# Performance work log

Measured on AMD Instinct MI355X. Metric: run time of the kernel, lower is better.

The kernel has to match this reference:

```python
import jax, jax.numpy as jnp
import numpy as np

N = 262144
IN_DIM = 1024
HID = 256
E = 16
TOP_K = 2


def setup_inputs() -> dict:
    key = jax.random.key(0)
    k1, k2, k3, k4, k5 = jax.random.split(key, 5)
    x = jax.random.normal(k1, (N, IN_DIM), dtype=jnp.float32)
    # Kaiming-ish init scaled for stability
    W1 = jax.random.normal(k2, (IN_DIM, HID), dtype=jnp.float32) * (1.0 / np.sqrt(IN_DIM))
    b1 = jnp.zeros((HID,), dtype=jnp.float32)
    W2 = jax.random.normal(k3, (HID, E), dtype=jnp.float32) * (1.0 / np.sqrt(HID))
    b2 = jnp.zeros((E,), dtype=jnp.float32)
    return {"x": x, "W1": W1, "b1": b1, "W2": W2, "b2": b2}


def reference(x, W1, b1, W2, b2):
    # MLP router: Linear -> ELU -> Linear
    h = jax.nn.elu(x @ W1 + b1)            # [N, HID]
    logits = h @ W2 + b2                   # [N, E]
    # top-k mask: keep top-k logits, set the rest to -inf (scatter semantics)
    vals, idx = jax.lax.top_k(logits, TOP_K)          # [N, K]
    rows = jnp.arange(logits.shape[0])[:, None]        # [N, 1]
    masked = jnp.full_like(logits, -jnp.inf).at[rows, idx].set(vals)
    alpha = jax.nn.softmax(masked, axis=-1)            # [N, E]
    return alpha, logits
```

## Files before the change

### kernel.cpp

```cpp
#include <hip/hip_runtime.h>
#include <math.h>

#define KDIM 1024
#define HID 256
#define NE 16
#define ROWS_BLK 128
#define KCH 32
#define NCHUNK 32
#define CH_BYTES 32768
#define W2T_PLANE (NE * HID)
#define ABUF(i) ((i) * 16384)
#define SMEM_BYTES 65536

typedef __attribute__((ext_vector_type(8))) _Float16 f16x8;
typedef __attribute__((ext_vector_type(16))) float f32x16;
typedef __attribute__((ext_vector_type(4))) float f32x4;

__global__ void prep_w1(const float* __restrict__ W1, _Float16* __restrict__ img) {
  int idx = blockIdx.x * 256 + threadIdx.x;
  int col = idx & 255, kgl = idx >> 8;
  int c = kgl >> 2, kg = kgl & 3, k8 = kgl * 8;
  f16x8 p1, p2;
#pragma unroll
  for (int i = 0; i < 8; ++i) {
    float v = W1[(size_t)(k8 + i) * HID + col];
    _Float16 a = (_Float16)v;
    _Float16 b = (_Float16)((v - (float)a) * 4096.0f);
    p1[i] = a; p2[i] = b;
  }
  size_t off = (size_t)c * 16384 + (size_t)kg * 2048 + (size_t)col * 8;
  *(f16x8*)(img + off) = p1;
  *(f16x8*)(img + off + 8192) = p2;
}

__global__ void prep_w2(const float* __restrict__ W2, _Float16* __restrict__ w2t) {
  int idx = blockIdx.x * 256 + threadIdx.x;
  int e = idx & 15, k = idx >> 4;
  float v = W2[(size_t)k * NE + e];
  _Float16 a = (_Float16)v;
  _Float16 b = (_Float16)((v - (float)a) * 4096.0f);
  w2t[(size_t)e * HID + k] = a;
  w2t[W2T_PLANE + (size_t)e * HID + k] = b;
}

__global__ __launch_bounds__(512, 2) void fused_router(
    const float* __restrict__ x, const _Float16* __restrict__ w1img,
    const _Float16* __restrict__ w2t, const float* __restrict__ bias1,
    const float* __restrict__ bias2, float* __restrict__ outA,
    float* __restrict__ outL)
{
  extern __shared__ char smem[];
  const int t = threadIdx.x, l = t & 63, w = t >> 6;
  const int rowg = w >> 2, colg = w & 3;
  const int l31 = l & 31, hi = l >> 5;
  const int R0 = blockIdx.x * ROWS_BLK;
  const int arow0 = rowg * 64 + l31;
  const int bcol0 = colg * 64 + l31;

  const int xr = t >> 2, xq = t & 3;
  const float* xbase = x + (size_t)(R0 + xr) * KDIM + xq * 8;

  const char* bimg = (const char*)w1img + (size_t)bcol0 * 16 + (size_t)hi * 4096;

  f32x16 acc0[2][2], accA[2][2];
#pragma unroll
  for (int rt = 0; rt < 2; ++rt)
#pragma unroll
    for (int ct = 0; ct < 2; ++ct)
#pragma unroll
      for (int j = 0; j < 16; ++j) { acc0[rt][ct][j] = 0.f; accA[rt][ct][j] = 0.f; }

  float xvA[8], xvB[8];
  f16x8 bsetA[8], bsetB[8];

#define XLOADV(XV_, C_) do {                                                  \
    *(float4*)(XV_)     = *(const float4*)(xbase + (size_t)(C_) * KCH);       \
    *(float4*)((XV_)+4) = *(const float4*)(xbase + (size_t)(C_) * KCH + 4);   \
  } while (0)

#define BLOADR(BS_, C_) do {                                                  \
    const char* bp_ = bimg + (size_t)(C_) * CH_BYTES;                         \
    _Pragma("unroll") for (int i_ = 0; i_ < 8; ++i_) {                        \
      const int off_ = ((i_ >> 2) & 1) * 8192 + ((i_ >> 1) & 1) * 512         \
                     + (i_ & 1) * 16384;                                      \
      BS_[i_] = *(const f16x8*)(bp_ + off_);                                  \
    }                                                                         \
  } while (0)

#define ASPLITV(XV_, ABW_) do {                                               \
    f16x8 pa_, pb_;                                                           \
    _Pragma("unroll") for (int j_ = 0; j_ < 8; ++j_) {                        \
      float v_ = (XV_)[j_];                                                   \
      _Float16 a_ = (_Float16)v_;                                             \
      _Float16 b_ = (_Float16)((v_ - (float)a_) * 4096.0f);                   \
      pa_[j_] = a_; pb_[j_] = b_;                                             \
    }                                                                         \
    int ao_ = ABUF(ABW_) + xq * 2048 + xr * 16;                               \
    *(f16x8*)(smem + ao_) = pa_;                                              \
    *(f16x8*)(smem + ao_ + 8192) = pb_;                                       \
  } while (0)

#define COMPUTE(AR_, BS_) do {                                                \
    _Pragma("unroll") for (int s_ = 0; s_ < 2; ++s_) {                        \
      const int gg_ = 2 * s_ + hi;                                            \
      f16x8 a1_[2], a2_[2];                                                   \
      _Pragma("unroll") for (int rt_ = 0; rt_ < 2; ++rt_) {                   \
        int ao_ = ABUF(AR_) + gg_ * 2048 + (arow0 + 32 * rt_) * 16;           \
        a1_[rt_] = *(const f16x8*)(smem + ao_);                               \
        a2_[rt_] = *(const f16x8*)(smem + ao_ + 8192);                        \
      }                                                                       \
      __builtin_amdgcn_s_setprio(1);                                          \
      _Pragma("unroll") for (int ct_ = 0; ct_ < 2; ++ct_)                     \
      _Pragma("unroll") for (int rt_ = 0; rt_ < 2; ++rt_)                     \
        acc0[rt_][ct_] = __builtin_amdgcn_mfma_f32_32x32x16_f16(              \
            a1_[rt_], BS_[4 * s_ + 2 * ct_ + 0], acc0[rt_][ct_], 0, 0, 0);    \
      _Pragma("unroll") for (int ct_ = 0; ct_ < 2; ++ct_)                     \
      _Pragma("unroll") for (int rt_ = 0; rt_ < 2; ++rt_)                     \
        accA[rt_][ct_] = __builtin_amdgcn_mfma_f32_32x32x16_f16(              \
            a1_[rt_], BS_[4 * s_ + 2 * ct_ + 1], accA[rt_][ct_], 0, 0, 0);    \
      _Pragma("unroll") for (int ct_ = 0; ct_ < 2; ++ct_)                     \
      _Pragma("unroll") for (int rt_ = 0; rt_ < 2; ++rt_)                     \
        accA[rt_][ct_] = __builtin_amdgcn_mfma_f32_32x32x16_f16(              \
            a2_[rt_], BS_[4 * s_ + 2 * ct_ + 0], accA[rt_][ct_], 0, 0, 0);    \
      __builtin_amdgcn_s_setprio(0);                                          \
    }                                                                         \
  } while (0)

#define BODY(C_, AR_, AW_, BCUR_, BNXT_, XC_, XL_) do {                       \
    if ((C_) + 1 < NCHUNK) BLOADR(BNXT_, (C_) + 1);                           \
    if ((C_) + 2 < NCHUNK) XLOADV(XL_, (C_) + 2);                             \
    if ((C_) + 1 < NCHUNK) ASPLITV(XC_, AW_);                                 \
    COMPUTE(AR_, BCUR_);                                                      \
    asm volatile("s_waitcnt lgkmcnt(0)" ::: "memory");                        \
    __builtin_amdgcn_s_barrier();                                             \
  } while (0)

  XLOADV(xvA, 0);
  BLOADR(bsetA, 0);
  XLOADV(xvB, 1);
  ASPLITV(xvA, 0);
  asm volatile("s_waitcnt lgkmcnt(0)" ::: "memory");
  __builtin_amdgcn_s_barrier();

#pragma unroll 1
  for (int cb = 0; cb < NCHUNK; cb += 2) {
    BODY(cb,     0, 1, bsetA, bsetB, xvB, xvA);
    BODY(cb + 1, 1, 0, bsetB, bsetA, xvA, xvB);
  }

  const float c12 = 1.0f / 4096.0f;
  const int tok = l & 15, g2 = l >> 4;

#pragma unroll 1
  for (int p = 0; p < 2; ++p) {
    __syncthreads();
    if (rowg == p) {
#pragma unroll
      for (int ct = 0; ct < 2; ++ct) {
        int col = bcol0 + 32 * ct;
        float bc = bias1[col];
        int cg = col >> 3, cb = (col & 7) * 2;
#pragma unroll
        for (int rt = 0; rt < 2; ++rt) {
#pragma unroll
          for (int r = 0; r < 16; ++r) {
            int tloc = 32 * rt + (r & 3) + 8 * (r >> 2) + 4 * hi;
            float v = acc0[rt][ct][r] + c12 * accA[rt][ct][r] + bc;
            v = v > 0.f ? v : expm1f(v);
            _Float16 h1 = (_Float16)v;
            _Float16 h2 = (_Float16)((v - (float)h1) * 4096.0f);
            int off = tloc * 512 + ((cg ^ (tloc & 7)) << 4) + cb;
            *(_Float16*)(smem + off) = h1;
            *(_Float16*)(smem + 32768 + off) = h2;
          }
        }
      }
    }
    __syncthreads();
    if (w < 4) {
      int tloc = w * 16 + tok;
      f32x4 L0, LA;
#pragma unroll
      for (int j = 0; j < 4; ++j) { L0[j] = 0.f; LA[j] = 0.f; }
      const _Float16* w2a = w2t + (size_t)tok * HID;
      const _Float16* w2b = w2a + W2T_PLANE;
#pragma unroll
      for (int kt = 0; kt < 8; ++kt) {
        int gg = (kt * 4 + g2) ^ (tloc & 7);
        f16x8 hb1 = *(const f16x8*)(smem + tloc * 512 + (gg << 4));
        f16x8 hb2 = *(const f16x8*)(smem + 32768 + tloc * 512 + (gg << 4));
        f16x8 wa = *(const f16x8*)(w2a + kt * 32 + 8 * g2);
        f16x8 wb = *(const f16x8*)(w2b + kt * 32 + 8 * g2);
        L0 = __builtin_amdgcn_mfma_f32_16x16x32_f16(wa, hb1, L0, 0, 0, 0);
        LA = __builtin_amdgcn_mfma_f32_16x16x32_f16(wa, hb2, LA, 0, 0, 0);
        LA = __builtin_amdgcn_mfma_f32_16x16x32_f16(wb, hb1, LA, 0, 0, 0);
      }
      float4 b2v = *(const float4*)(bias2 + 4 * g2);
      float L[4];
      L[0] = L0[0] + c12 * LA[0] + b2v.x;
      L[1] = L0[1] + c12 * LA[1] + b2v.y;
      L[2] = L0[2] + c12 * LA[2] + b2v.z;
      L[3] = L0[3] + c12 * LA[3] + b2v.w;

      float o1[4], o2[4], o3[4];
#pragma unroll
      for (int j = 0; j < 4; ++j) o1[j] = __shfl_xor(L[j], 16);
#pragma unroll
      for (int j = 0; j < 4; ++j) o2[j] = __shfl_xor(L[j], 32);
#pragma unroll
      for (int j = 0; j < 4; ++j) o3[j] = __shfl_xor(o1[j], 32);

      float all16[16];
#pragma unroll
      for (int cq = 0; cq < 4; ++cq) {
        int xg = cq ^ g2;
#pragma unroll
        for (int j = 0; j < 4; ++j) {
          float v = L[j];
          v = (xg == 1) ? o1[j] : v;
          v = (xg == 2) ? o2[j] : v;
          v = (xg == 3) ? o3[j] : v;
          all16[cq * 4 + j] = v;
        }
      }

      int i1 = 0; float m1 = all16[0];
#pragma unroll
      for (int e = 1; e < 16; ++e) { if (all16[e] > m1) { m1 = all16[e]; i1 = e; } }
      int i2 = -1; float m2 = -INFINITY;
#pragma unroll
      for (int e = 0; e < 16; ++e) { if (e != i1 && all16[e] > m2) { m2 = all16[e]; i2 = e; } }
      float ex = expf(m2 - m1);
      float sden = 1.f + ex;
      float A1 = 1.f / sden;
      float A2 = ex / sden;

      int e0 = 4 * g2;
      float4 alv;
      alv.x = (e0 + 0 == i1) ? A1 : ((e0 + 0 == i2) ? A2 : 0.f);
      alv.y = (e0 + 1 == i1) ? A1 : ((e0 + 1 == i2) ? A2 : 0.f);
      alv.z = (e0 + 2 == i1) ? A1 : ((e0 + 2 == i2) ? A2 : 0.f);
      alv.w = (e0 + 3 == i1) ? A1 : ((e0 + 3 == i2) ? A2 : 0.f);

      size_t orow = (size_t)(R0 + p * 64 + tloc);
      float4 lgv; lgv.x = L[0]; lgv.y = L[1]; lgv.z = L[2]; lgv.w = L[3];
      *(float4*)(outL + orow * NE + e0) = lgv;
      *(float4*)(outA + orow * NE + e0) = alv;
    }
  }
#undef XLOADV
#undef BLOADR
#undef ASPLITV
#undef COMPUTE
#undef BODY
}

extern "C" void kernel_launch(void* const* d_in, const int* in_sizes, int n_in,
                              void* d_out, int out_size, void* d_ws, size_t ws_size,
                              hipStream_t stream) {
  const float* x  = (const float*)d_in[0];
  const float* W1 = (const float*)d_in[1];
  const float* b1 = (const float*)d_in[2];
  const float* W2 = (const float*)d_in[3];
  const float* b2 = (const float*)d_in[4];
  _Float16* w1img = (_Float16*)d_ws;
  _Float16* w2t = w1img + (size_t)NCHUNK * (CH_BYTES / 2);
  float* outA = (float*)d_out;
  const size_t n_tok = (size_t)in_sizes[0] / KDIM;
  float* outL = outA + n_tok * NE;

  prep_w1<<<dim3(128), dim3(256), 0, stream>>>(W1, w1img);
  prep_w2<<<dim3(16), dim3(256), 0, stream>>>(W2, w2t);

  hipFuncSetAttribute((const void*)fused_router,
                      hipFuncAttributeMaxDynamicSharedMemorySize, SMEM_BYTES);
  fused_router<<<dim3((unsigned)(n_tok / ROWS_BLK)), dim3(512), SMEM_BYTES, stream>>>(
      x, w1img, w2t, b1, b2, outA, outL);
}
```

Before: 642.1 us.

## Shrink router block tile to 32 rows with 256 threads for higher occupancy

Result: slower. 706.6 us (+10.0%).

```diff
diff --git a/kernel.cpp b/kernel.cpp
--- a/kernel.cpp
+++ b/kernel.cpp
@@ -4,14 +4,15 @@
 #define KDIM 1024
 #define HID 256
 #define NE 16
-#define ROWS_BLK 128
+#define ROWS_BLK 32
 #define KCH 32
 #define NCHUNK 32
 #define CH_BYTES 32768
 #define W2T_PLANE (NE * HID)
-#define ABUF(i) ((i) * 16384)
-#define SMEM_BYTES 65536
-
+#define ABUF(i) ((i) * 4096)
+#define SMEM_BYTES 32768
+
+typedef __attribute__((ext_vector_type(4))) _Float16 f16x4;
 typedef __attribute__((ext_vector_type(8))) _Float16 f16x8;
 typedef __attribute__((ext_vector_type(16))) float f32x16;
 typedef __attribute__((ext_vector_type(4))) float f32x4;
@@ -43,7 +44,7 @@
   w2t[W2T_PLANE + (size_t)e * HID + k] = b;
 }
 
-__global__ __launch_bounds__(512, 2) void fused_router(
+__global__ __launch_bounds__(256, 3) void fused_router(
     const float* __restrict__ x, const _Float16* __restrict__ w1img,
     const _Float16* __restrict__ w2t, const float* __restrict__ bias1,
     const float* __restrict__ bias2, float* __restrict__ outA,
@@ -51,31 +52,27 @@
 {
   extern __shared__ char smem[];
   const int t = threadIdx.x, l = t & 63, w = t >> 6;
-  const int rowg = w >> 2, colg = w & 3;
   const int l31 = l & 31, hi = l >> 5;
   const int R0 = blockIdx.x * ROWS_BLK;
-  const int arow0 = rowg * 64 + l31;
-  const int bcol0 = colg * 64 + l31;
-
-  const int xr = t >> 2, xq = t & 3;
-  const float* xbase = x + (size_t)(R0 + xr) * KDIM + xq * 8;
+  const int bcol0 = w * 64 + l31;
+
+  const int xrow = t & 31, xq = t >> 5;
+  const int xkg = xq >> 1, xhalf = xq & 1;
+  const float* xbase = x + (size_t)(R0 + xrow) * KDIM + xkg * 8 + xhalf * 4;
 
   const char* bimg = (const char*)w1img + (size_t)bcol0 * 16 + (size_t)hi * 4096;
 
-  f32x16 acc0[2][2], accA[2][2];
-#pragma unroll
-  for (int rt = 0; rt < 2; ++rt)
-#pragma unroll
-    for (int ct = 0; ct < 2; ++ct)
-#pragma unroll
-      for (int j = 0; j < 16; ++j) { acc0[rt][ct][j] = 0.f; accA[rt][ct][j] = 0.f; }
-
-  float xvA[8], xvB[8];
+  f32x16 acc0[2], accA[2];
+#pragma unroll
+  for (int ct = 0; ct < 2; ++ct)
+#pragma unroll
+    for (int j = 0; j < 16; ++j) { acc0[ct][j] = 0.f; accA[ct][j] = 0.f; }
+
+  float4 xvA, xvB;
   f16x8 bsetA[8], bsetB[8];
 
 #define XLOADV(XV_, C_) do {                                                  \
-    *(float4*)(XV_)     = *(const float4*)(xbase + (size_t)(C_) * KCH);       \
-    *(float4*)((XV_)+4) = *(const float4*)(xbase + (size_t)(C_) * KCH + 4);   \
+    XV_ = *(const float4*)(xbase + (size_t)(C_) * KCH);                       \
   } while (0)
 
 #define BLOADR(BS_, C_) do {                                                  \
@@ -88,40 +85,35 @@
   } while (0)
 
 #define ASPLITV(XV_, ABW_) do {                                               \
-    f16x8 pa_, pb_;                                                           \
-    _Pragma("unroll") for (int j_ = 0; j_ < 8; ++j_) {                        \
-      float v_ = (XV_)[j_];                                                   \
+    float vals_[4] = {(XV_).x, (XV_).y, (XV_).z, (XV_).w};                    \
+    f16x4 pa_, pb_;                                                           \
+    _Pragma("unroll") for (int j_ = 0; j_ < 4; ++j_) {                        \
+      float v_ = vals_[j_];                                                   \
       _Float16 a_ = (_Float16)v_;                                             \
       _Float16 b_ = (_Float16)((v_ - (float)a_) * 4096.0f);                   \
       pa_[j_] = a_; pb_[j_] = b_;                                             \
     }                                                                         \
-    int ao_ = ABUF(ABW_) + xq * 2048 + xr * 16;                               \
-    *(f16x8*)(smem + ao_) = pa_;                                              \
-    *(f16x8*)(smem + ao_ + 8192) = pb_;                                       \
+    int ao_ = ABUF(ABW_) + xkg * 512 + xrow * 16 + xhalf * 8;                 \
+    *(f16x4*)(smem + ao_) = pa_;                                              \
+    *(f16x4*)(smem + ao_ + 2048) = pb_;                                       \
   } while (0)
 
 #define COMPUTE(AR_, BS_) do {                                                \
     _Pragma("unroll") for (int s_ = 0; s_ < 2; ++s_) {                        \
       const int gg_ = 2 * s_ + hi;                                            \
-      f16x8 a1_[2], a2_[2];                                                   \
-      _Pragma("unroll") for (int rt_ = 0; rt_ < 2; ++rt_) {                   \
-        int ao_ = ABUF(AR_) + gg_ * 2048 + (arow0 + 32 * rt_) * 16;           \
-        a1_[rt_] = *(const f16x8*)(smem + ao_);                               \
-        a2_[rt_] = *(const f16x8*)(smem + ao_ + 8192);                        \
-      }                                                                       \
+      int ao_ = ABUF(AR_) + gg_ * 512 + l31 * 16;                             \
+      f16x8 a1_ = *(const f16x8*)(smem + ao_);                                \
+      f16x8 a2_ = *(const f16x8*)(smem + ao_ + 2048);                         \
       __builtin_amdgcn_s_setprio(1);                                          \
       _Pragma("unroll") for (int ct_ = 0; ct_ < 2; ++ct_)                     \
-      _Pragma("unroll") for (int rt_ = 0; rt_ < 2; ++rt_)                     \
-        acc0[rt_][ct_] = __builtin_amdgcn_mfma_f32_32x32x16_f16(              \
-            a1_[rt_], BS_[4 * s_ + 2 * ct_ + 0], acc0[rt_][ct_], 0, 0, 0);    \
+        acc0[ct_] = __builtin_amdgcn_mfma_f32_32x32x16_f16(                   \
+            a1_, BS_[4 * s_ + 2 * ct_ + 0], acc0[ct_], 0, 0, 0);              \
       _Pragma("unroll") for (int ct_ = 0; ct_ < 2; ++ct_)                     \
-      _Pragma("unroll") for (int rt_ = 0; rt_ < 2; ++rt_)                     \
-        accA[rt_][ct_] = __builtin_amdgcn_mfma_f32_32x32x16_f16(              \
-            a1_[rt_], BS_[4 * s_ + 2 * ct_ + 1], accA[rt_][ct_], 0, 0, 0);    \
+        accA[ct_] = __builtin_amdgcn_mfma_f32_32x32x16_f16(                   \
+            a1_, BS_[4 * s_ + 2 * ct_ + 1], accA[ct_], 0, 0, 0);              \
       _Pragma("unroll") for (int ct_ = 0; ct_ < 2; ++ct_)                     \
-      _Pragma("unroll") for (int rt_ = 0; rt_ < 2; ++rt_)                     \
-        accA[rt_][ct_] = __builtin_amdgcn_mfma_f32_32x32x16_f16(              \
-            a2_[rt_], BS_[4 * s_ + 2 * ct_ + 0], accA[rt_][ct_], 0, 0, 0);    \
+        accA[ct_] = __builtin_amdgcn_mfma_f32_32x32x16_f16(                   \
+            a2_, BS_[4 * s_ + 2 * ct_ + 0], accA[ct_], 0, 0, 0);              \
       __builtin_amdgcn_s_setprio(0);                                          \
     }                                                                         \
   } while (0)
@@ -151,102 +143,95 @@
   const float c12 = 1.0f / 4096.0f;
   const int tok = l & 15, g2 = l >> 4;
 
-#pragma unroll 1
-  for (int p = 0; p < 2; ++p) {
-    __syncthreads();
-    if (rowg == p) {
-#pragma unroll
-      for (int ct = 0; ct < 2; ++ct) {
-        int col = bcol0 + 32 * ct;
-        float bc = bias1[col];
-        int cg = col >> 3, cb = (col & 7) * 2;
-#pragma unroll
-        for (int rt = 0; rt < 2; ++rt) {
-#pragma unroll
-          for (int r = 0; r < 16; ++r) {
-            int tloc = 32 * rt + (r & 3) + 8 * (r >> 2) + 4 * hi;
-            float v = acc0[rt][ct][r] + c12 * accA[rt][ct][r] + bc;
-            v = v > 0.f ? v : expm1f(v);
-            _Float16 h1 = (_Float16)v;
-            _Float16 h2 = (_Float16)((v - (float)h1) * 4096.0f);
-            int off = tloc * 512 + ((cg ^ (tloc & 7)) << 4) + cb;
-            *(_Float16*)(smem + off) = h1;
-            *(_Float16*)(smem + 32768 + off) = h2;
-          }
-        }
+  __syncthreads();
+#pragma unroll
+  for (int ct = 0; ct < 2; ++ct) {
+    int col = bcol0 + 32 * ct;
+    float bc = bias1[col];
+    int cg = col >> 3, cb = (col & 7) * 2;
+#pragma unroll
+    for (int r = 0; r < 16; ++r) {
+      int tloc = (r & 3) + 8 * (r >> 2) + 4 * hi;
+      float v = acc0[ct][r] + c12 * accA[ct][r] + bc;
+      v = v > 0.f ? v : expm1f(v);
+      _Float16 h1 = (_Float16)v;
+      _Float16 h2 = (_Float16)((v - (float)h1) * 4096.0f);
+      int off = tloc * 512 + ((cg ^ (tloc & 7)) << 4) + cb;
+      *(_Float16*)(smem + off) = h1;
+      *(_Float16*)(smem + 16384 + off) = h2;
+    }
+  }
+  __syncthreads();
+
+  if (w < 2) {
+    int tloc = w * 16 + tok;
+    f32x4 L0, LA;
+#pragma unroll
+    for (int j = 0; j < 4; ++j) { L0[j] = 0.f; LA[j] = 0.f; }
+    const _Float16* w2a = w2t + (size_t)tok * HID;
+    const _Float16* w2b = w2a + W2T_PLANE;
+#pragma unroll
+    for (int kt = 0; kt < 8; ++kt) {
+      int gg = (kt * 4 + g2) ^ (tloc & 7);
+      f16x8 hb1 = *(const f16x8*)(smem + tloc * 512 + (gg << 4));
+      f16x8 hb2 = *(const f16x8*)(smem + 16384 + tloc * 512 + (gg << 4));
+      f16x8 wa = *(const f16x8*)(w2a + kt * 32 + 8 * g2);
+      f16x8 wb = *(const f16x8*)(w2b + kt * 32 + 8 * g2);
+      L0 = __builtin_amdgcn_mfma_f32_16x16x32_f16(wa, hb1, L0, 0, 0, 0);
+      LA = __builtin_amdgcn_mfma_f32_16x16x32_f16(wa, hb2, LA, 0, 0, 0);
+      LA = __builtin_amdgcn_mfma_f32_16x16x32_f16(wb, hb1, LA, 0, 0, 0);
+    }
+    float4 b2v = *(const float4*)(bias2 + 4 * g2);
+    float L[4];
+    L[0] = L0[0] + c12 * LA[0] + b2v.x;
+    L[1] = L0[1] + c12 * LA[1] + b2v.y;
+    L[2] = L0[2] + c12 * LA[2] + b2v.z;
+    L[3] = L0[3] + c12 * LA[3] + b2v.w;
+
+    float o1[4], o2[4], o3[4];
+#pragma unroll
+    for (int j = 0; j < 4; ++j) o1[j] = __shfl_xor(L[j], 16);
+#pragma unroll
+    for (int j = 0; j < 4; ++j) o2[j] = __shfl_xor(L[j], 32);
+#pragma unroll
+    for (int j = 0; j < 4; ++j) o3[j] = __shfl_xor(o1[j], 32);
+
+    float all16[16];
+#pragma unroll
+    for (int cq = 0; cq < 4; ++cq) {
+      int xg = cq ^ g2;
+#pragma unroll
+      for (int j = 0; j < 4; ++j) {
+        float v = L[j];
+        v = (xg == 1) ? o1[j] : v;
+        v = (xg == 2) ? o2[j] : v;
+        v = (xg == 3) ? o3[j] : v;
+        all16[cq * 4 + j] = v;
       }
     }
-    __syncthreads();
-    if (w < 4) {
-      int tloc = w * 16 + tok;
-      f32x4 L0, LA;
-#pragma unroll
-      for (int j = 0; j < 4; ++j) { L0[j] = 0.f; LA[j] = 0.f; }
-      const _Float16* w2a = w2t + (size_t)tok * HID;
-      const _Float16* w2b = w2a + W2T_PLANE;
-#pragma unroll
-      for (int kt = 0; kt < 8; ++kt) {
-        int gg = (kt * 4 + g2) ^ (tloc & 7);
-        f16x8 hb1 = *(const f16x8*)(smem + tloc * 512 + (gg << 4));
-        f16x8 hb2 = *(const f16x8*)(smem + 32768 + tloc * 512 + (gg << 4));
-        f16x8 wa = *(const f16x8*)(w2a + kt * 32 + 8 * g2);
-        f16x8 wb = *(const f16x8*)(w2b + kt * 32 + 8 * g2);
-        L0 = __builtin_amdgcn_mfma_f32_16x16x32_f16(wa, hb1, L0, 0, 0, 0);
-        LA = __builtin_amdgcn_mfma_f32_16x16x32_f16(wa, hb2, LA, 0, 0, 0);
-        LA = __builtin_amdgcn_mfma_f32_16x16x32_f16(wb, hb1, LA, 0, 0, 0);
-      }
-      float4 b2v = *(const float4*)(bias2 + 4 * g2);
-      float L[4];
-      L[0] = L0[0] + c12 * LA[0] + b2v.x;
-      L[1] = L0[1] + c12 * LA[1] + b2v.y;
-      L[2] = L0[2] + c12 * LA[2] + b2v.z;
-      L[3] = L0[3] + c12 * LA[3] + b2v.w;
-
-      float o1[4], o2[4], o3[4];
-#pragma unroll
-      for (int j = 0; j < 4; ++j) o1[j] = __shfl_xor(L[j], 16);
-#pragma unroll
-      for (int j = 0; j < 4; ++j) o2[j] = __shfl_xor(L[j], 32);
-#pragma unroll
-      for (int j = 0; j < 4; ++j) o3[j] = __shfl_xor(o1[j], 32);
-
-      float all16[16];
-#pragma unroll
-      for (int cq = 0; cq < 4; ++cq) {
-        int xg = cq ^ g2;
-#pragma unroll
-        for (int j = 0; j < 4; ++j) {
-          float v = L[j];
-          v = (xg == 1) ? o1[j] : v;
-          v = (xg == 2) ? o2[j] : v;
-          v = (xg == 3) ? o3[j] : v;
-          all16[cq * 4 + j] = v;
-        }
-      }
-
-      int i1 = 0; float m1 = all16[0];
-#pragma unroll
-      for (int e = 1; e < 16; ++e) { if (all16[e] > m1) { m1 = all16[e]; i1 = e; } }
-      int i2 = -1; float m2 = -INFINITY;
-#pragma unroll
-      for (int e = 0; e < 16; ++e) { if (e != i1 && all16[e] > m2) { m2 = all16[e]; i2 = e; } }
-      float ex = expf(m2 - m1);
-      float sden = 1.f + ex;
-      float A1 = 1.f / sden;
-      float A2 = ex / sden;
-
-      int e0 = 4 * g2;
-      float4 alv;
-      alv.x = (e0 + 0 == i1) ? A1 : ((e0 + 0 == i2) ? A2 : 0.f);
-      alv.y = (e0 + 1 == i1) ? A1 : ((e0 + 1 == i2) ? A2 : 0.f);
-      alv.z = (e0 + 2 == i1) ? A1 : ((e0 + 2 == i2) ? A2 : 0.f);
-      alv.w = (e0 + 3 == i1) ? A1 : ((e0 + 3 == i2) ? A2 : 0.f);
-
-      size_t orow = (size_t)(R0 + p * 64 + tloc);
-      float4 lgv; lgv.x = L[0]; lgv.y = L[1]; lgv.z = L[2]; lgv.w = L[3];
-      *(float4*)(outL + orow * NE + e0) = lgv;
-      *(float4*)(outA + orow * NE + e0) = alv;
-    }
+
+    int i1 = 0; float m1 = all16[0];
+#pragma unroll
+    for (int e = 1; e < 16; ++e) { if (all16[e] > m1) { m1 = all16[e]; i1 = e; } }
+    int i2 = -1; float m2 = -INFINITY;
+#pragma unroll
+    for (int e = 0; e < 16; ++e) { if (e != i1 && all16[e] > m2) { m2 = all16[e]; i2 = e; } }
+    float ex = expf(m2 - m1);
+    float sden = 1.f + ex;
+    float A1 = 1.f / sden;
+    float A2 = ex / sden;
+
+    int e0 = 4 * g2;
+    float4 alv;
+    alv.x = (e0 + 0 == i1) ? A1 : ((e0 + 0 == i2) ? A2 : 0.f);
+    alv.y = (e0 + 1 == i1) ? A1 : ((e0 + 1 == i2) ? A2 : 0.f);
+    alv.z = (e0 + 2 == i1) ? A1 : ((e0 + 2 == i2) ? A2 : 0.f);
+    alv.w = (e0 + 3 == i1) ? A1 : ((e0 + 3 == i2) ? A2 : 0.f);
+
+    size_t orow = (size_t)(R0 + tloc);
+    float4 lgv; lgv.x = L[0]; lgv.y = L[1]; lgv.z = L[2]; lgv.w = L[3];
+    *(float4*)(outL + orow * NE + e0) = lgv;
+    *(float4*)(outA + orow * NE + e0) = alv;
   }
 #undef XLOADV
 #undef BLOADR
@@ -274,6 +259,6 @@
 
   hipFuncSetAttribute((const void*)fused_router,
                       hipFuncAttributeMaxDynamicSharedMemorySize, SMEM_BYTES);
-  fused_router<<<dim3((unsigned)(n_tok / ROWS_BLK)), dim3(512), SMEM_BYTES, stream>>>(
+  fused_router<<<dim3((unsigned)(n_tok / ROWS_BLK)), dim3(256), SMEM_BYTES, stream>>>(
       x, w1img, w2t, b1, b2, outA, outL);
 }
```
